# Kernel tuning notes

Hardware: AMD Instinct MI355X
Metric: run time of the kernel (lower is better)

Reference implementation:

```python
import jax, jax.numpy as jnp
import numpy as np
from math import sqrt

B, S, D_MODEL = 2, 2048, 1024
H = 16
ADIM = D_MODEL // H  # 64
K_REL = 16
N_PEMB = 2 * K_REL + 1  # 33, bidirectional rel-pos vocabulary


def setup_inputs() -> dict:
    key = jax.random.key(0)
    ks = jax.random.split(key, 8)
    sc = 0.02
    return {
        "iQ": jax.random.normal(ks[0], (B, S, D_MODEL), jnp.float32),
        "iK": jax.random.normal(ks[1], (B, S, D_MODEL), jnp.float32),
        "iV": jax.random.normal(ks[2], (B, S, D_MODEL), jnp.float32),
        "Wq": jax.random.normal(ks[3], (D_MODEL, D_MODEL), jnp.float32) * sc,
        "Wk": jax.random.normal(ks[4], (D_MODEL, D_MODEL), jnp.float32) * sc,
        "Wv": jax.random.normal(ks[5], (D_MODEL, D_MODEL), jnp.float32) * sc,
        "Wo": jax.random.normal(ks[6], (D_MODEL, D_MODEL), jnp.float32) * sc,
        "rel_pemb": jax.random.normal(ks[7], (N_PEMB, ADIM), jnp.float32) * sc,
    }


def reference(iQ, iK, iV, Wq, Wk, Wv, Wo, rel_pemb):
    b, nq, _ = iQ.shape
    seql = iK.shape[1]
    # projections -> [b, h, len, d]
    q = (iQ @ Wq).reshape(b, nq, H, ADIM).transpose(0, 2, 1, 3)
    k = (iK @ Wk).reshape(b, seql, H, ADIM).transpose(0, 2, 1, 3)
    v = (iV @ Wv).reshape(b, seql, H, ADIM).transpose(0, 2, 1, 3)
    # content scores: [b, h, nq, seql]
    scores = jnp.einsum("bhqd,bhsd->bhqs", q, k)
    # relative position bias: rel[i, j] = clamp(j - i, -K, K) + K
    pos = jnp.arange(seql)
    rel = jnp.clip(pos[None, :] - pos[:, None], -K_REL, K_REL) + K_REL
    rel = rel[seql - nq:, :]  # narrow to query rows: [nq, seql]
    e = rel_pemb[rel]  # [nq, seql, d]
    scores = scores + jnp.einsum("bhqd,qsd->bhqs", q, e)
    scores = scores / sqrt(ADIM)
    attn = jax.nn.softmax(scores, axis=-1)
    ctx = jnp.einsum("bhqs,bhsd->bqhd", attn, v).reshape(b, nq, H * ADIM)
    return ctx @ Wo
```

## Files before the change

kernel.cpp:

```cpp
#include <hip/hip_runtime.h>
#include <hip/hip_bf16.h>

#define BB 2
#define S 2048
#define DM 1024
#define H 16
#define ADIM 64
#define NP 33

typedef __bf16 bf16x8 __attribute__((ext_vector_type(8)));
typedef float f32x4 __attribute__((ext_vector_type(4)));

__device__ __forceinline__ void gload16(const void* g, void* l) {
  __builtin_amdgcn_global_load_lds(
      (__attribute__((address_space(1))) void*)(g),
      (__attribute__((address_space(3))) void*)(l), 16, 0, 0);
}

__global__ __launch_bounds__(256) void tobf16(
    const float* __restrict__ X0, const float* __restrict__ X1,
    const float* __restrict__ X2, __bf16* __restrict__ Y0,
    __bf16* __restrict__ Y1, __bf16* __restrict__ Y2) {
  const float* X; __bf16* Y;
  switch (blockIdx.z) {
    case 0: X = X0; Y = Y0; break;
    case 1: X = X1; Y = Y1; break;
    default: X = X2; Y = Y2; break;
  }
  size_t i = ((size_t)blockIdx.x * 256 + threadIdx.x) * 8;
  float4 a0 = *(const float4*)(X + i);
  float4 a1 = *(const float4*)(X + i + 4);
  bf16x8 v;
  v[0] = (__bf16)a0.x; v[1] = (__bf16)a0.y;
  v[2] = (__bf16)a0.z; v[3] = (__bf16)a0.w;
  v[4] = (__bf16)a1.x; v[5] = (__bf16)a1.y;
  v[6] = (__bf16)a1.z; v[7] = (__bf16)a1.w;
  *(bf16x8*)(Y + i) = v;
}

__global__ __launch_bounds__(256) void wtrans(
    const float* __restrict__ W0, const float* __restrict__ W1,
    const float* __restrict__ W2, __bf16* __restrict__ T0,
    __bf16* __restrict__ T1, __bf16* __restrict__ T2) {
  const float* W; __bf16* T;
  switch (blockIdx.z) {
    case 0: W = W0; T = T0; break;
    case 1: W = W1; T = T1; break;
    default: W = W2; T = T2; break;
  }
  __shared__ __bf16 tile[64][65];
  int j = threadIdx.x & 63, i0 = threadIdx.x >> 6;
  int n0 = blockIdx.x * 64, k0 = blockIdx.y * 64;
#pragma unroll
  for (int p = 0; p < 16; ++p) {
    int i = i0 + p * 4;
    tile[i][j] = (__bf16)W[(size_t)(k0 + i) * DM + n0 + j];
  }
  __syncthreads();
#pragma unroll
  for (int p = 0; p < 16; ++p) {
    int i = i0 + p * 4;
    T[(size_t)(n0 + i) * DM + k0 + j] = tile[j][i];
  }
}

#define LDK 40
template <bool A_FP32, int BN, typename CT>
__device__ __forceinline__ void gemm_body(const void* __restrict__ Av,
                                          const __bf16* __restrict__ BT,
                                          CT* __restrict__ C, int mode,
                                          int m0, int n0) {
  constexpr int NF = BN / 32;
  constexpr int BH = BN / 16;
  __shared__ __align__(16) __bf16 As[128 * LDK];
  __shared__ __align__(16) __bf16 Bs[BN * 32];
  int t = threadIdx.x;
  int w = t >> 6, lane = t & 63, l15 = lane & 15, quad = lane >> 4;
  int wm = w >> 1, wn = w & 1;
  constexpr int LA = A_FP32 ? LDK : 32;
  f32x4 acc[4][NF] = {};
  int lr = t >> 2;
  int lk = (t & 3) * 8;
  int r4 = lane >> 2;
  int c8 = (lane & 3) * 8;
  for (int k0 = 0; k0 < DM; k0 += 32) {
    if constexpr (A_FP32) {
#pragma unroll
      for (int rr = 0; rr < 2; ++rr) {
        int row = rr * 64 + lr;
        const float* src = (const float*)Av + (size_t)(m0 + row) * DM + k0 + lk;
        float4 a0 = *(const float4*)src;
        float4 a1 = *(const float4*)(src + 4);
        bf16x8 v;
        v[0] = (__bf16)a0.x; v[1] = (__bf16)a0.y;
        v[2] = (__bf16)a0.z; v[3] = (__bf16)a0.w;
        v[4] = (__bf16)a1.x; v[5] = (__bf16)a1.y;
        v[6] = (__bf16)a1.z; v[7] = (__bf16)a1.w;
        *(bf16x8*)&As[row * LDK + lk] = v;
      }
    } else {
#pragma unroll
      for (int q = 0; q < 2; ++q) {
        int half = w * 2 + q;
        gload16((const __bf16*)Av + (size_t)(m0 + half * 16 + r4) * DM + k0 + c8,
                &As[half * 512]);
      }
    }
#pragma unroll
    for (int q = 0; q < BH / 4; ++q) {
      int half = w * (BH / 4) + q;
      gload16(&BT[(size_t)(n0 + half * 16 + r4) * DM + k0 + c8],
              &Bs[half * 512]);
    }
    __syncthreads();
    bf16x8 af[4], bfr[NF];
#pragma unroll
    for (int mi = 0; mi < 4; ++mi)
      af[mi] = *(const bf16x8*)&As[(wm * 64 + mi * 16 + l15) * LA + quad * 8];
#pragma unroll
    for (int ni = 0; ni < NF; ++ni)
      bfr[ni] =
          *(const bf16x8*)&Bs[(wn * (BN / 2) + ni * 16 + l15) * 32 + quad * 8];
#pragma unroll
    for (int mi = 0; mi < 4; ++mi)
#pragma unroll
      for (int ni = 0; ni < NF; ++ni)
        acc[mi][ni] = __builtin_amdgcn_mfma_f32_16x16x32_bf16(
            af[mi], bfr[ni], acc[mi][ni], 0, 0, 0);
    __syncthreads();
  }
#pragma unroll
  for (int mi = 0; mi < 4; ++mi)
#pragma unroll
    for (int ni = 0; ni < NF; ++ni)
#pragma unroll
      for (int r = 0; r < 4; ++r) {
        int row = m0 + wm * 64 + mi * 16 + quad * 4 + r;
        int col = n0 + wn * (BN / 2) + ni * 16 + l15;
        CT v = (CT)acc[mi][ni][r];
        if (mode == 0) {
          C[(size_t)row * DM + col] = v;
        } else if (mode == 3) {
          int hh = row >> 6, dd = row & (ADIM - 1);
          int bb = col >> 11, ss = col & (S - 1);
          C[((size_t)(bb * H + hh) * ADIM + dd) * S + ss] = v;
        } else {
          int b = row >> 11, s = row & (S - 1);
          int h = col >> 6, d = col & (ADIM - 1);
          if (mode == 1)
            C[((size_t)(b * H + h) * S + s) * ADIM + d] = v;
          else
            C[((size_t)(b * H + h) * ADIM + d) * S + s] = v;
        }
      }
}

__global__ __launch_bounds__(256) void proj3(
    const float* __restrict__ iQ, const float* __restrict__ iK,
    const float* __restrict__ iV, const __bf16* __restrict__ WqT,
    const __bf16* __restrict__ WkT, const __bf16* __restrict__ WvT,
    __bf16* __restrict__ Qw, __bf16* __restrict__ Kw,
    __bf16* __restrict__ Vt) {
  const float* A; const __bf16* B; __bf16* C; int mode;
  switch (blockIdx.z) {
    case 0: A = iQ; B = WqT; C = Qw; mode = 1; break;
    case 1: A = iK; B = WkT; C = Kw; mode = 1; break;
    default: A = iV; B = WvT; C = Vt; mode = 2; break;
  }
  int i2 = blockIdx.x + (blockIdx.y << 3);
  int xcd = i2 & 7, slot = i2 >> 3;
  int m0 = (xcd + ((slot >> 3) << 3)) * 128;
  int n0 = (slot & 7) * 128;
  gemm_body<true, 128, __bf16>(A, B, C, mode, m0, n0);
}

__global__ __launch_bounds__(256) void proj2b(
    const __bf16* __restrict__ Qb, const __bf16* __restrict__ Kb,
    const __bf16* __restrict__ WqT, const __bf16* __restrict__ WkT,
    __bf16* __restrict__ Qw, __bf16* __restrict__ Kw) {
  const __bf16* A; const __bf16* B; __bf16* C;
  if (blockIdx.z == 0) { A = Qb; B = WqT; C = Qw; }
  else                 { A = Kb; B = WkT; C = Kw; }
  int i2 = blockIdx.x + (blockIdx.y << 3);
  int xcd = i2 & 7, slot = i2 >> 3;
  int m0 = (xcd + ((slot >> 3) << 3)) * 128;
  int n0 = (slot & 7) * 128;
  gemm_body<false, 128, __bf16>(A, B, C, 1, m0, n0);
}

__global__ __launch_bounds__(256) void projV(
    const __bf16* __restrict__ WvT, const __bf16* __restrict__ Vb,
    __bf16* __restrict__ Vt) {
  int m0 = blockIdx.y * 128;
  int n0 = blockIdx.x * 128;
  gemm_body<false, 128, __bf16>(WvT, Vb, Vt, 3, m0, n0);
}

__global__ __launch_bounds__(256) void gemm_final(
    const __bf16* __restrict__ ctx, const __bf16* __restrict__ WoT,
    float* __restrict__ out) {
  int i2 = blockIdx.x + (blockIdx.y << 4);
  int xcd = i2 & 7, slot = i2 >> 3;
  int m0 = ((xcd << 2) + (slot >> 4)) * 128;
  int n0 = (slot & 15) * 64;
  gemm_body<false, 64, float>(ctx, WoT, out, 0, m0, n0);
}

#define AST 72
__global__ __launch_bounds__(256) void attn_flash(
    const __bf16* __restrict__ Qw, const __bf16* __restrict__ Kw,
    const __bf16* __restrict__ Vt, const float* __restrict__ pemb,
    __bf16* __restrict__ ctx) {
  int i = blockIdx.x + (blockIdx.y << 5);
  int a = i & 7, j = i >> 3;
  int bh = (a << 2) + (j >> 5);
  int q0 = (j & 31) * 64;
  int b = bh >> 4, h = bh & 15;
  int t = threadIdx.x, w = t >> 6, lane = t & 63, l15 = lane & 15,
      quad = lane >> 4;
  const __bf16* Qh = Qw + (size_t)bh * S * ADIM;
  const __bf16* Kh = Kw + (size_t)bh * S * ADIM;
  const __bf16* Vh = Vt + (size_t)bh * ADIM * S;

  __shared__ __align__(16) char smem[36352];
  __bf16* Ks = (__bf16*)smem;
  __bf16* Vs = (__bf16*)(smem + 9216);
  float* pband = (float*)(smem + 18432);
  __bf16* pbufw = (__bf16*)(smem + 27136 + w * 2304);
  __bf16* peb = (__bf16*)smem;

  for (int ii = t; ii < 48 * 64; ii += 256) {
    int r = ii >> 6, d = ii & 63;
    peb[r * AST + d] = (r < NP) ? (__bf16)pemb[ii] : (__bf16)0.f;
  }

  int qa = q0 + w * 16 + l15;
  bf16x8 qf0 = *(const bf16x8*)&Qh[(size_t)qa * ADIM + quad * 8];
  bf16x8 qf1 = *(const bf16x8*)&Qh[(size_t)qa * ADIM + 32 + quad * 8];
  __syncthreads();

  {
    f32x4 pc[3] = {};
#pragma unroll
    for (int ni = 0; ni < 3; ++ni) {
      bf16x8 b0 = *(const bf16x8*)&peb[(ni * 16 + l15) * AST + quad * 8];
      bf16x8 b1 = *(const bf16x8*)&peb[(ni * 16 + l15) * AST + 32 + quad * 8];
      pc[ni] = __builtin_amdgcn_mfma_f32_16x16x32_bf16(qf0, b0, pc[ni], 0, 0, 0);
      pc[ni] = __builtin_amdgcn_mfma_f32_16x16x32_bf16(qf1, b1, pc[ni], 0, 0, 0);
    }
#pragma unroll
    for (int ni = 0; ni < 3; ++ni)
#pragma unroll
      for (int r = 0; r < 4; ++r) {
        int col = ni * 16 + l15;
        if (col < NP) pband[(w * 16 + quad * 4 + r) * 34 + col] = pc[ni][r];
      }
  }
  __syncthreads();

  int qc = q0 + w * 16 + quad * 4;
  int lrow = w * 16 + quad * 4;
  int qw0 = q0 + w * 16;
  float lsum[4] = {0.f, 0.f, 0.f, 0.f};
  f32x4 o[4] = {};

  float pb0[4], pb32[4];
#pragma unroll
  for (int r = 0; r < 4; ++r) {
    pb0[r] = pband[(lrow + r) * 34 + 0] * 0.125f;
    pb32[r] = pband[(lrow + r) * 34 + 32] * 0.125f;
  }

  int srow = t >> 3;
  int scol = (t & 7) * 8;
  bf16x8 k0r = *(const bf16x8*)&Kh[(size_t)srow * ADIM + scol];
  bf16x8 k1r = *(const bf16x8*)&Kh[(size_t)(32 + srow) * ADIM + scol];
  bf16x8 v0r = *(const bf16x8*)&Vh[(size_t)srow * S + scol];
  bf16x8 v1r = *(const bf16x8*)&Vh[(size_t)(32 + srow) * S + scol];

  for (int s0 = 0; s0 < S; s0 += 64) {
    __syncthreads();
    *(bf16x8*)&Ks[srow * AST + scol] = k0r;
    *(bf16x8*)&Ks[(32 + srow) * AST + scol] = k1r;
    *(bf16x8*)&Vs[srow * AST + scol] = v0r;
    *(bf16x8*)&Vs[(32 + srow) * AST + scol] = v1r;
    int sn = s0 + 64;
    if (sn < S) {
      k0r = *(const bf16x8*)&Kh[(size_t)(sn + srow) * ADIM + scol];
      k1r = *(const bf16x8*)&Kh[(size_t)(sn + 32 + srow) * ADIM + scol];
      v0r = *(const bf16x8*)&Vh[(size_t)srow * S + sn + scol];
      v1r = *(const bf16x8*)&Vh[(size_t)(32 + srow) * S + sn + scol];
    }
    __syncthreads();

    f32x4 c[4];
#pragma unroll
    for (int jj = 0; jj < 4; ++jj) {
      f32x4 cj = {};
      bf16x8 kb0 = *(const bf16x8*)&Ks[(jj * 16 + l15) * AST + quad * 8];
      bf16x8 kb1 = *(const bf16x8*)&Ks[(jj * 16 + l15) * AST + 32 + quad * 8];
      cj = __builtin_amdgcn_mfma_f32_16x16x32_bf16(qf0, kb0, cj, 0, 0, 0);
      cj = __builtin_amdgcn_mfma_f32_16x16x32_bf16(qf1, kb1, cj, 0, 0, 0);
      c[jj] = cj;
    }

    float pv[4][4];
    bool below = (s0 + 79 <= qw0);
    bool above = (s0 >= qw0 + 31);
    if (below || above) {
#pragma unroll
      for (int jj = 0; jj < 4; ++jj)
#pragma unroll
        for (int r = 0; r < 4; ++r) {
          float pb = below ? pb0[r] : pb32[r];
          float e = __expf(__builtin_fmaf(c[jj][r], 0.125f, pb));
          lsum[r] += e;
          pv[jj][r] = e;
        }
    } else {
#pragma unroll
      for (int jj = 0; jj < 4; ++jj)
#pragma unroll
        for (int r = 0; r < 4; ++r) {
          int qg = qc + r;
          int sg = s0 + jj * 16 + l15;
          int i0 = sg - qg; i0 = i0 < -16 ? -16 : (i0 > 16 ? 16 : i0); i0 += 16;
          float e = __expf((c[jj][r] + pband[(lrow + r) * 34 + i0]) * 0.125f);
          lsum[r] += e;
          pv[jj][r] = e;
        }
    }

#pragma unroll
    for (int jj = 0; jj < 4; ++jj)
#pragma unroll
      for (int r = 0; r < 4; ++r)
        pbufw[(quad * 4 + r) * AST + jj * 16 + l15] = (__bf16)pv[jj][r];
    bf16x8 pa0 = *(const bf16x8*)&pbufw[l15 * AST + quad * 8];
    bf16x8 pa1 = *(const bf16x8*)&pbufw[l15 * AST + 32 + quad * 8];

#pragma unroll
    for (int nt = 0; nt < 4; ++nt) {
      bf16x8 vb0 = *(const bf16x8*)&Vs[(nt * 16 + l15) * AST + quad * 8];
      bf16x8 vb1 = *(const bf16x8*)&Vs[(nt * 16 + l15) * AST + 32 + quad * 8];
      o[nt] = __builtin_amdgcn_mfma_f32_16x16x32_bf16(pa0, vb0, o[nt], 0, 0, 0);
      o[nt] = __builtin_amdgcn_mfma_f32_16x16x32_bf16(pa1, vb1, o[nt], 0, 0, 0);
    }
  }

#pragma unroll
  for (int r = 0; r < 4; ++r) {
#pragma unroll
    for (int mm = 1; mm < 16; mm <<= 1) lsum[r] += __shfl_xor(lsum[r], mm, 64);
  }
#pragma unroll
  for (int nt = 0; nt < 4; ++nt)
#pragma unroll
    for (int r = 0; r < 4; ++r) {
      int qg = qc + r;
      int d = nt * 16 + l15;
      ctx[(size_t)(b * S + qg) * DM + h * ADIM + d] =
          (__bf16)(o[nt][r] / lsum[r]);
    }
}

extern "C" void kernel_launch(void* const* d_in, const int* in_sizes, int n_in,
                              void* d_out, int out_size, void* d_ws,
                              size_t ws_size, hipStream_t stream) {
  bool sizes_ok =
      (n_in == 8 && in_sizes[0] == BB * S * DM && in_sizes[1] == BB * S * DM &&
       in_sizes[2] == BB * S * DM && in_sizes[3] == DM * DM &&
       in_sizes[4] == DM * DM && in_sizes[5] == DM * DM &&
       in_sizes[6] == DM * DM && in_sizes[7] == NP * ADIM &&
       out_size == BB * S * DM);
  if (!sizes_ok) return;
  if (ws_size < 33ull * 1024 * 1024) return;

  const float* iQ = (const float*)d_in[0];
  const float* iK = (const float*)d_in[1];
  const float* iV = (const float*)d_in[2];
  const float* Wq = (const float*)d_in[3];
  const float* Wk = (const float*)d_in[4];
  const float* Wv = (const float*)d_in[5];
  const float* Wo = (const float*)d_in[6];
  const float* pemb = (const float*)d_in[7];

  char* w = (char*)d_ws;
  const size_t MB = 1024 * 1024;
  __bf16* Qw  = (__bf16*)(w + 0 * MB);
  __bf16* Kw  = (__bf16*)(w + 8 * MB);
  __bf16* Vt  = (__bf16*)(w + 16 * MB);
  __bf16* ctx = (__bf16*)(w + 24 * MB);
  __bf16* WqT = (__bf16*)(w + 24 * MB);
  __bf16* WkT = (__bf16*)(w + 26 * MB);
  __bf16* WvT = (__bf16*)(w + 28 * MB);
  __bf16* WoT = (__bf16*)(w + 0 * MB);

  wtrans<<<dim3(16, 16, 3), 256, 0, stream>>>(Wq, Wk, Wv, WqT, WkT, WvT);
  if (ws_size >= 56ull * 1024 * 1024) {
    __bf16* Qb = (__bf16*)(w + 32 * MB);
    __bf16* Kb = (__bf16*)(w + 40 * MB);
    __bf16* Vb = (__bf16*)(w + 48 * MB);
    tobf16<<<dim3(2048, 1, 3), 256, 0, stream>>>(iQ, iK, iV, Qb, Kb, Vb);
    proj2b<<<dim3(8, 32, 2), 256, 0, stream>>>(Qb, Kb, WqT, WkT, Qw, Kw);
    projV<<<dim3(32, 8), 256, 0, stream>>>(WvT, Vb, Vt);
  } else {
    proj3<<<dim3(8, 32, 3), 256, 0, stream>>>(iQ, iK, iV, WqT, WkT, WvT,
                                              Qw, Kw, Vt);
  }
  attn_flash<<<dim3(S / 64, BB * H), 256, 0, stream>>>(Qw, Kw, Vt, pemb, ctx);
  wtrans<<<dim3(16, 16, 1), 256, 0, stream>>>(Wo, Wo, Wo, WoT, WoT, WoT);
  gemm_final<<<dim3(16, 32), 256, 0, stream>>>(ctx, WoT, (float*)d_out);
}
```

Measured before the change: 259.8 us.

## Swizzle attention LDS tiles, transpose QK MFMA, and merge Q/K/V projection launches

The attention kernel drops the padded LDS stride of 72 in favour of an XOR-swizzled 64-wide layout for the K, V and P tiles, which shrinks shared memory and is meant to avoid bank conflicts. It also swaps the MFMA operands for QK^T so each lane owns one query row. That lets the row sum accumulate in a single scalar per lane, reducing shuffle reductions and per-row bias bookkeeping. The P tile is now written as packed 4-wide vectors instead of scalar stores. Separately, the Q/K and V projection kernels are merged into a single launch with z=3, trading one kernel launch for branch divergence by block index.

```diff
diff --git a/kernel.cpp b/kernel.cpp
--- a/kernel.cpp
+++ b/kernel.cpp
@@ -9,6 +9,7 @@
 #define NP 33
 
 typedef __bf16 bf16x8 __attribute__((ext_vector_type(8)));
+typedef __bf16 bf16x4 __attribute__((ext_vector_type(4)));
 typedef float f32x4 __attribute__((ext_vector_type(4)));
 
 __device__ __forceinline__ void gload16(const void* g, void* l) {
@@ -174,26 +175,26 @@
   gemm_body<true, 128, __bf16>(A, B, C, mode, m0, n0);
 }
 
-__global__ __launch_bounds__(256) void proj2b(
+__global__ __launch_bounds__(256) void proj3b(
     const __bf16* __restrict__ Qb, const __bf16* __restrict__ Kb,
-    const __bf16* __restrict__ WqT, const __bf16* __restrict__ WkT,
-    __bf16* __restrict__ Qw, __bf16* __restrict__ Kw) {
-  const __bf16* A; const __bf16* B; __bf16* C;
-  if (blockIdx.z == 0) { A = Qb; B = WqT; C = Qw; }
-  else                 { A = Kb; B = WkT; C = Kw; }
+    const __bf16* __restrict__ Vb, const __bf16* __restrict__ WqT,
+    const __bf16* __restrict__ WkT, const __bf16* __restrict__ WvT,
+    __bf16* __restrict__ Qw, __bf16* __restrict__ Kw,
+    __bf16* __restrict__ Vt) {
   int i2 = blockIdx.x + (blockIdx.y << 3);
-  int xcd = i2 & 7, slot = i2 >> 3;
-  int m0 = (xcd + ((slot >> 3) << 3)) * 128;
-  int n0 = (slot & 7) * 128;
-  gemm_body<false, 128, __bf16>(A, B, C, 1, m0, n0);
-}
-
-__global__ __launch_bounds__(256) void projV(
-    const __bf16* __restrict__ WvT, const __bf16* __restrict__ Vb,
-    __bf16* __restrict__ Vt) {
-  int m0 = blockIdx.y * 128;
-  int n0 = blockIdx.x * 128;
-  gemm_body<false, 128, __bf16>(WvT, Vb, Vt, 3, m0, n0);
+  if (blockIdx.z == 2) {
+    int m0 = (i2 & 7) * 128;
+    int n0 = (i2 >> 3) * 128;
+    gemm_body<false, 128, __bf16>(WvT, Vb, Vt, 3, m0, n0);
+  } else {
+    const __bf16* A; const __bf16* B; __bf16* C;
+    if (blockIdx.z == 0) { A = Qb; B = WqT; C = Qw; }
+    else                 { A = Kb; B = WkT; C = Kw; }
+    int xcd = i2 & 7, slot = i2 >> 3;
+    int m0 = (xcd + ((slot >> 3) << 3)) * 128;
+    int n0 = (slot & 7) * 128;
+    gemm_body<false, 128, __bf16>(A, B, C, 1, m0, n0);
+  }
 }
 
 __global__ __launch_bounds__(256) void gemm_final(
@@ -206,7 +207,7 @@
   gemm_body<false, 64, float>(ctx, WoT, out, 0, m0, n0);
 }
 
-#define AST 72
+#define SWZ(row, sl) (((row) << 6) + ((((sl) ^ ((row) & 7))) << 3))
 __global__ __launch_bounds__(256) void attn_flash(
     const __bf16* __restrict__ Qw, const __bf16* __restrict__ Kw,
     const __bf16* __restrict__ Vt, const float* __restrict__ pemb,
@@ -222,16 +223,16 @@
   const __bf16* Kh = Kw + (size_t)bh * S * ADIM;
   const __bf16* Vh = Vt + (size_t)bh * ADIM * S;
 
-  __shared__ __align__(16) char smem[36352];
+  __shared__ __align__(16) char smem[33280];
   __bf16* Ks = (__bf16*)smem;
-  __bf16* Vs = (__bf16*)(smem + 9216);
-  float* pband = (float*)(smem + 18432);
-  __bf16* pbufw = (__bf16*)(smem + 27136 + w * 2304);
+  __bf16* Vs = (__bf16*)(smem + 8192);
+  float* pband = (float*)(smem + 16384);
+  __bf16* pbufw = (__bf16*)(smem + 25088 + w * 2048);
   __bf16* peb = (__bf16*)smem;
 
   for (int ii = t; ii < 48 * 64; ii += 256) {
     int r = ii >> 6, d = ii & 63;
-    peb[r * AST + d] = (r < NP) ? (__bf16)pemb[ii] : (__bf16)0.f;
+    peb[r * 64 + d] = (r < NP) ? (__bf16)pemb[ii] : (__bf16)0.f;
   }
 
   int qa = q0 + w * 16 + l15;
@@ -243,8 +244,8 @@
     f32x4 pc[3] = {};
 #pragma unroll
     for (int ni = 0; ni < 3; ++ni) {
-      bf16x8 b0 = *(const bf16x8*)&peb[(ni * 16 + l15) * AST + quad * 8];
-      bf16x8 b1 = *(const bf16x8*)&peb[(ni * 16 + l15) * AST + 32 + quad * 8];
+      bf16x8 b0 = *(const bf16x8*)&peb[(ni * 16 + l15) * 64 + quad * 8];
+      bf16x8 b1 = *(const bf16x8*)&peb[(ni * 16 + l15) * 64 + 32 + quad * 8];
       pc[ni] = __builtin_amdgcn_mfma_f32_16x16x32_bf16(qf0, b0, pc[ni], 0, 0, 0);
       pc[ni] = __builtin_amdgcn_mfma_f32_16x16x32_bf16(qf1, b1, pc[ni], 0, 0, 0);
     }
@@ -258,21 +259,19 @@
   }
   __syncthreads();
 
+  int qg = q0 + w * 16 + l15;
   int qc = q0 + w * 16 + quad * 4;
-  int lrow = w * 16 + quad * 4;
   int qw0 = q0 + w * 16;
-  float lsum[4] = {0.f, 0.f, 0.f, 0.f};
+  const float* pbrow = pband + (w * 16 + l15) * 34;
+  float lsum = 0.f;
   f32x4 o[4] = {};
 
-  float pb0[4], pb32[4];
-#pragma unroll
-  for (int r = 0; r < 4; ++r) {
-    pb0[r] = pband[(lrow + r) * 34 + 0] * 0.125f;
-    pb32[r] = pband[(lrow + r) * 34 + 32] * 0.125f;
-  }
+  float pb0s = pbrow[0] * 0.125f;
+  float pb32s = pbrow[32] * 0.125f;
 
   int srow = t >> 3;
-  int scol = (t & 7) * 8;
+  int sslot = t & 7;
+  int scol = sslot * 8;
   bf16x8 k0r = *(const bf16x8*)&Kh[(size_t)srow * ADIM + scol];
   bf16x8 k1r = *(const bf16x8*)&Kh[(size_t)(32 + srow) * ADIM + scol];
   bf16x8 v0r = *(const bf16x8*)&Vh[(size_t)srow * S + scol];
@@ -280,10 +279,10 @@
 
   for (int s0 = 0; s0 < S; s0 += 64) {
     __syncthreads();
-    *(bf16x8*)&Ks[srow * AST + scol] = k0r;
-    *(bf16x8*)&Ks[(32 + srow) * AST + scol] = k1r;
-    *(bf16x8*)&Vs[srow * AST + scol] = v0r;
-    *(bf16x8*)&Vs[(32 + srow) * AST + scol] = v1r;
+    *(bf16x8*)&Ks[SWZ(srow, sslot)] = k0r;
+    *(bf16x8*)&Ks[SWZ(32 + srow, sslot)] = k1r;
+    *(bf16x8*)&Vs[SWZ(srow, sslot)] = v0r;
+    *(bf16x8*)&Vs[SWZ(32 + srow, sslot)] = v1r;
     int sn = s0 + 64;
     if (sn < S) {
       k0r = *(const bf16x8*)&Kh[(size_t)(sn + srow) * ADIM + scol];
@@ -297,10 +296,11 @@
 #pragma unroll
     for (int jj = 0; jj < 4; ++jj) {
       f32x4 cj = {};
-      bf16x8 kb0 = *(const bf16x8*)&Ks[(jj * 16 + l15) * AST + quad * 8];
-      bf16x8 kb1 = *(const bf16x8*)&Ks[(jj * 16 + l15) * AST + 32 + quad * 8];
-      cj = __builtin_amdgcn_mfma_f32_16x16x32_bf16(qf0, kb0, cj, 0, 0, 0);
-      cj = __builtin_amdgcn_mfma_f32_16x16x32_bf16(qf1, kb1, cj, 0, 0, 0);
+      int krow = jj * 16 + l15;
+      bf16x8 kb0 = *(const bf16x8*)&Ks[SWZ(krow, quad)];
+      bf16x8 kb1 = *(const bf16x8*)&Ks[SWZ(krow, 4 + quad)];
+      cj = __builtin_amdgcn_mfma_f32_16x16x32_bf16(kb0, qf0, cj, 0, 0, 0);
+      cj = __builtin_amdgcn_mfma_f32_16x16x32_bf16(kb1, qf1, cj, 0, 0, 0);
       c[jj] = cj;
     }
 
@@ -308,13 +308,13 @@
     bool below = (s0 + 79 <= qw0);
     bool above = (s0 >= qw0 + 31);
     if (below || above) {
+      float pb = below ? pb0s : pb32s;
 #pragma unroll
       for (int jj = 0; jj < 4; ++jj)
 #pragma unroll
         for (int r = 0; r < 4; ++r) {
-          float pb = below ? pb0[r] : pb32[r];
           float e = __expf(__builtin_fmaf(c[jj][r], 0.125f, pb));
-          lsum[r] += e;
+          lsum += e;
           pv[jj][r] = e;
         }
     } else {
@@ -322,45 +322,48 @@
       for (int jj = 0; jj < 4; ++jj)
 #pragma unroll
         for (int r = 0; r < 4; ++r) {
-          int qg = qc + r;
-          int sg = s0 + jj * 16 + l15;
+          int sg = s0 + jj * 16 + quad * 4 + r;
           int i0 = sg - qg; i0 = i0 < -16 ? -16 : (i0 > 16 ? 16 : i0); i0 += 16;
-          float e = __expf((c[jj][r] + pband[(lrow + r) * 34 + i0]) * 0.125f);
-          lsum[r] += e;
+          float e = __expf((c[jj][r] + pbrow[i0]) * 0.125f);
+          lsum += e;
           pv[jj][r] = e;
         }
     }
 
 #pragma unroll
-    for (int jj = 0; jj < 4; ++jj)
-#pragma unroll
-      for (int r = 0; r < 4; ++r)
-        pbufw[(quad * 4 + r) * AST + jj * 16 + l15] = (__bf16)pv[jj][r];
-    bf16x8 pa0 = *(const bf16x8*)&pbufw[l15 * AST + quad * 8];
-    bf16x8 pa1 = *(const bf16x8*)&pbufw[l15 * AST + 32 + quad * 8];
+    for (int jj = 0; jj < 4; ++jj) {
+      bf16x4 pw;
+      pw[0] = (__bf16)pv[jj][0]; pw[1] = (__bf16)pv[jj][1];
+      pw[2] = (__bf16)pv[jj][2]; pw[3] = (__bf16)pv[jj][3];
+      int sl = (2 * jj + (quad >> 1)) ^ (l15 & 7);
+      *(bf16x4*)&pbufw[(l15 << 6) + (sl << 3) + (quad & 1) * 4] = pw;
+    }
+    bf16x8 pa0 = *(const bf16x8*)&pbufw[SWZ(l15, quad)];
+    bf16x8 pa1 = *(const bf16x8*)&pbufw[SWZ(l15, 4 + quad)];
 
 #pragma unroll
     for (int nt = 0; nt < 4; ++nt) {
-      bf16x8 vb0 = *(const bf16x8*)&Vs[(nt * 16 + l15) * AST + quad * 8];
-      bf16x8 vb1 = *(const bf16x8*)&Vs[(nt * 16 + l15) * AST + 32 + quad * 8];
+      int vrow = nt * 16 + l15;
+      bf16x8 vb0 = *(const bf16x8*)&Vs[SWZ(vrow, quad)];
+      bf16x8 vb1 = *(const bf16x8*)&Vs[SWZ(vrow, 4 + quad)];
       o[nt] = __builtin_amdgcn_mfma_f32_16x16x32_bf16(pa0, vb0, o[nt], 0, 0, 0);
       o[nt] = __builtin_amdgcn_mfma_f32_16x16x32_bf16(pa1, vb1, o[nt], 0, 0, 0);
     }
   }
 
-#pragma unroll
-  for (int r = 0; r < 4; ++r) {
-#pragma unroll
-    for (int mm = 1; mm < 16; mm <<= 1) lsum[r] += __shfl_xor(lsum[r], mm, 64);
-  }
+  lsum += __shfl_xor(lsum, 16, 64);
+  lsum += __shfl_xor(lsum, 32, 64);
+  float ls[4];
+#pragma unroll
+  for (int r = 0; r < 4; ++r) ls[r] = __shfl(lsum, quad * 4 + r, 64);
 #pragma unroll
   for (int nt = 0; nt < 4; ++nt)
 #pragma unroll
     for (int r = 0; r < 4; ++r) {
-      int qg = qc + r;
+      int qq = qc + r;
       int d = nt * 16 + l15;
-      ctx[(size_t)(b * S + qg) * DM + h * ADIM + d] =
-          (__bf16)(o[nt][r] / lsum[r]);
+      ctx[(size_t)(b * S + qq) * DM + h * ADIM + d] =
+          (__bf16)(o[nt][r] / ls[r]);
     }
 }
 
@@ -402,8 +405,8 @@
     __bf16* Kb = (__bf16*)(w + 40 * MB);
     __bf16* Vb = (__bf16*)(w + 48 * MB);
     tobf16<<<dim3(2048, 1, 3), 256, 0, stream>>>(iQ, iK, iV, Qb, Kb, Vb);
-    proj2b<<<dim3(8, 32, 2), 256, 0, stream>>>(Qb, Kb, WqT, WkT, Qw, Kw);
-    projV<<<dim3(32, 8), 256, 0, stream>>>(WvT, Vb, Vt);
+    proj3b<<<dim3(8, 32, 3), 256, 0, stream>>>(Qb, Kb, Vb, WqT, WkT, WvT,
+                                               Qw, Kw, Vt);
   } else {
     proj3<<<dim3(8, 32, 3), 256, 0, stream>>>(iQ, iK, iV, WqT, WkT, WvT,
                                               Qw, Kw, Vt);
```

New measurement: 241.9 us. 1.07x faster.
